# Performance work log

Measured on AMD Instinct MI355X. Metric: run time of the kernel, lower is better.

Reference implementation:

```python
import jax, jax.numpy as jnp
import numpy as np

NUM_HEADS = 16
HIDDEN = 1024
EPS = 1e-5


def _layernorm(x, g, b):
    mu = jnp.mean(x, axis=-1, keepdims=True)
    var = jnp.mean((x - mu) ** 2, axis=-1, keepdims=True)
    return (x - mu) * jax.lax.rsqrt(var + EPS) * g + b


def setup_inputs() -> dict:
    key = jax.random.key(0)
    ks = jax.random.split(key, 10)
    B, S, H = 2, 2048, HIDDEN
    s = 0.02
    d = {
        "X": jax.random.normal(ks[0], (B, S, H), jnp.float32),
        "Wq": jax.random.normal(ks[1], (H, H), jnp.float32) * s,
        "bq": jnp.zeros((H,), jnp.float32),
        "Wk": jax.random.normal(ks[2], (H, H), jnp.float32) * s,
        "bk": jnp.zeros((H,), jnp.float32),
        "Wv": jax.random.normal(ks[3], (H, H), jnp.float32) * s,
        "bv": jnp.zeros((H,), jnp.float32),
        "Wo": jax.random.normal(ks[4], (H, H), jnp.float32) * s,
        "bo": jnp.zeros((H,), jnp.float32),
        "ln1_g": jnp.ones((H,), jnp.float32),
        "ln1_b": jnp.zeros((H,), jnp.float32),
        "Wup": jax.random.normal(ks[5], (4 * H, H), jnp.float32) * s,
        "bup": jnp.zeros((4 * H,), jnp.float32),
        "Wdown": jax.random.normal(ks[6], (H, 4 * H), jnp.float32) * s,
        "bdown": jnp.zeros((H,), jnp.float32),
        "ln2_g": jnp.ones((H,), jnp.float32),
        "ln2_b": jnp.zeros((H,), jnp.float32),
    }
    return d


def reference(X, Wq, bq, Wk, bk, Wv, bv, Wo, bo, ln1_g, ln1_b,
              Wup, bup, Wdown, bdown, ln2_g, ln2_b):
    B, S, H = X.shape
    nh = NUM_HEADS
    hd = H // nh
    # QKV projections -> [B, nh, S, hd]
    q = (X @ Wq.T + bq).reshape(B, S, nh, hd).transpose(0, 2, 1, 3)
    k = (X @ Wk.T + bk).reshape(B, S, nh, hd).transpose(0, 2, 1, 3)
    v = (X @ Wv.T + bv).reshape(B, S, nh, hd).transpose(0, 2, 1, 3)
    scores = jnp.einsum("bhqd,bhkd->bhqk", q, k) / jnp.sqrt(jnp.float32(hd))
    causal = jnp.tril(jnp.ones((S, S), dtype=bool))
    scores = jnp.where(causal, scores, jnp.float32(-1e20))
    att = jax.nn.softmax(scores, axis=-1)  # dropout p=0 (eval)
    mid = jnp.einsum("bhqk,bhkd->bhqd", att, v)  # [B, nh, S, hd]
    mid = mid.transpose(0, 2, 1, 3).reshape(B, S, H)
    att_out = mid @ Wo.T + bo
    h = _layernorm(X + att_out, ln1_g, ln1_b)
    up = jax.nn.relu(h @ Wup.T + bup)
    down = up @ Wdown.T + bdown
    return _layernorm(h + down, ln2_g, ln2_b)
```

## Files before the change

### kernel.cpp

```cpp
#include <hip/hip_runtime.h>

#define B_ 2
#define S_ 2048
#define H_ 1024
#define NH 16
#define HD 64
#define LN_EPS 1e-5f

typedef unsigned short u16;
typedef unsigned int u32;
typedef __attribute__((ext_vector_type(8))) short bf16x8;
typedef __attribute__((ext_vector_type(4))) float f32x4;
typedef __attribute__((ext_vector_type(16))) float f32x16;
typedef __attribute__((ext_vector_type(4))) u32 u32x4;
typedef __attribute__((ext_vector_type(4))) u16 u16x4;

__device__ __forceinline__ u16 f2bf(float f) {
  u32 u = __float_as_uint(f);
  u32 r = (u + 0x7FFFu + ((u >> 16) & 1u)) >> 16;
  return (u16)r;
}
__device__ __forceinline__ float bflo(u32 w) { return __uint_as_float(w << 16); }
__device__ __forceinline__ float bfhi(u32 w) { return __uint_as_float(w & 0xffff0000u); }

__device__ __forceinline__ void gload_lds16(const void* g, void* l) {
  __builtin_amdgcn_global_load_lds(
      (const __attribute__((address_space(1))) void*)(uintptr_t)g,
      (__attribute__((address_space(3))) void*)(uintptr_t)l, 16, 0, 0);
}

__global__ __launch_bounds__(256) void k_cvt_all(const float* __restrict__ X,
                                                 const float* __restrict__ Wq,
                                                 const float* __restrict__ Wk,
                                                 const float* __restrict__ Wv,
                                                 const float* __restrict__ Wo,
                                                 const float* __restrict__ Wup,
                                                 const float* __restrict__ Wdn,
                                                 u16* __restrict__ dst) {
  const int i = blockIdx.x * 256 + threadIdx.x;
  const float* s;
  int off;
  if (i < 1048576)      { s = X;   off = 0; }
  else if (i < 1310720) { s = Wq;  off = 1048576; }
  else if (i < 1572864) { s = Wk;  off = 1310720; }
  else if (i < 1835008) { s = Wv;  off = 1572864; }
  else if (i < 2097152) { s = Wo;  off = 1835008; }
  else if (i < 3145728) { s = Wup; off = 2097152; }
  else                  { s = Wdn; off = 3145728; }
  f32x4 v = ((const f32x4*)s)[i - off];
  u16x4 o = { f2bf(v[0]), f2bf(v[1]), f2bf(v[2]), f2bf(v[3]) };
  ((u16x4*)dst)[i] = o;
}

__global__ __launch_bounds__(256) void k_pack3(const float* __restrict__ a,
                                               const float* __restrict__ b,
                                               const float* __restrict__ c,
                                               float* __restrict__ o) {
  int i = blockIdx.x * 256 + threadIdx.x;
  if (i >= 3 * H_) return;
  o[i] = (i < H_) ? a[i] : (i < 2 * H_ ? b[i - H_] : c[i - 2 * H_]);
}

template<int RELU, int F32OUT, int BF16OUT, int BIAS>
__global__ __launch_bounds__(512, 2) void k_gemm8(const u16* __restrict__ A,
                                                  const u16* __restrict__ W,
                                                  const float* __restrict__ bias,
                                                  float* __restrict__ outf,
                                                  u16* __restrict__ outb,
                                                  int M, int N, int lda, int ldb,
                                                  int Kc, int tilesM) {
  extern __shared__ u16 lds[];
  const int tid = threadIdx.x, lane = tid & 63, wid = tid >> 6;
  const int wr = wid >> 2, wc = wid & 3;
  const int lr = lane & 15, lk = lane >> 4;

  const int nwg = gridDim.x;
  const int bid = blockIdx.x;
  const int lid = (bid & 7) * (nwg >> 3) + (bid >> 3);
  const int ty = lid % tilesM;
  const int txz = lid / tilesM;
  const int tilesN = N >> 8;
  const int tx = txz % tilesN;
  const int kz = txz / tilesN;
  const int row0 = ty << 8, col0 = tx << 8;
  A += (size_t)kz * Kc;
  W += (size_t)kz * Kc;
  const size_t outoff = (size_t)kz * M * N;

  const int NT = Kc >> 6;

  f32x4 acc[8][4];
#pragma unroll
  for (int i = 0; i < 8; ++i)
#pragma unroll
    for (int j = 0; j < 4; ++j) acc[i][j] = (f32x4){0.f, 0.f, 0.f, 0.f};

  const int srow = tid >> 3;
  const int csw8 = ((tid & 7) ^ (srow & 7)) << 3;

  auto stage_ht = [&](int ht) {
    const int t = ht >> 2, sel = ht & 3;
    const int mat = (sel < 2) ? 1 : 0;
    const int hh = sel & 1;
    const u16* g = mat ? W : A;
    const int ld = mat ? ldb : lda;
    const int b0 = mat ? col0 : row0;
    const int kt = t << 6;
    u16* dst = lds + ((t & 1) << 15) + (mat << 14) + (hh << 13) + tid * 8;
#pragma unroll
    for (int j = 0; j < 2; ++j) {
      const int r = (hh << 7) + (j << 6) + srow;
      gload_lds16(g + (size_t)(b0 + r) * ld + kt + csw8, dst + (j << 12));
    }
  };

  union UU { u32x4 u; bf16x8 b; };
  auto ldvec = [&](const u16* base, int r, int c) -> bf16x8 {
    UU x;
    x.u = *(const u32x4*)(base + r * 64 + ((c ^ (r & 7)) << 3));
    return x.b;
  };

#pragma unroll
  for (int i = 0; i < 4; ++i) stage_ht(i);
  asm volatile("s_waitcnt vmcnt(0)" ::: "memory");
  __builtin_amdgcn_s_barrier();

  for (int t = 0; t < NT; ++t) {
    const u16* SA = lds + ((t & 1) << 15);
    const u16* SB = SA + 16384;
#pragma unroll
    for (int ph = 0; ph < 4; ++ph) {
      const int mh = ph >> 1, ks = ph & 1;
      const int c = (ks << 2) + lk;
      bf16x8 bb[4], aa[4];
#pragma unroll
      for (int ni = 0; ni < 4; ++ni)
        bb[ni] = ldvec(SB, (wc << 6) + (ni << 4) + lr, c);
#pragma unroll
      for (int mi = 0; mi < 4; ++mi)
        aa[mi] = ldvec(SA, (wr << 7) + (mh << 6) + (mi << 4) + lr, c);
      if (t + 1 < NT && ph < 2) {
        stage_ht(4 * (t + 1) + 2 * ph);
        stage_ht(4 * (t + 1) + 2 * ph + 1);
      }
      __builtin_amdgcn_s_barrier();
      __builtin_amdgcn_s_setprio(1);
#pragma unroll
      for (int mi = 0; mi < 4; ++mi)
#pragma unroll
        for (int ni = 0; ni < 4; ++ni)
          acc[(mh << 2) + mi][ni] = __builtin_amdgcn_mfma_f32_16x16x32_bf16(
              aa[mi], bb[ni], acc[(mh << 2) + mi][ni], 0, 0, 0);
      __builtin_amdgcn_s_setprio(0);
      if (ph == 3)
        asm volatile("s_waitcnt vmcnt(0)" ::: "memory");
      __builtin_amdgcn_s_barrier();
    }
  }

  float bs[4] = {0.f, 0.f, 0.f, 0.f};
  if (BIAS) {
#pragma unroll
    for (int ni = 0; ni < 4; ++ni)
      bs[ni] = bias[col0 + (wc << 6) + (ni << 4) + lr];
  }
#pragma unroll
  for (int mi = 0; mi < 8; ++mi) {
#pragma unroll
    for (int ni = 0; ni < 4; ++ni) {
#pragma unroll
      for (int r = 0; r < 4; ++r) {
        int row = row0 + (wr << 7) + (mi << 4) + (lk << 2) + r;
        int col = col0 + (wc << 6) + (ni << 4) + lr;
        float v = acc[mi][ni][r] + bs[ni];
        if (RELU) v = fmaxf(v, 0.f);
        if (F32OUT) outf[outoff + (size_t)row * N + col] = v;
        if (BF16OUT) outb[outoff + (size_t)row * N + col] = f2bf(v);
      }
    }
  }
}

__global__ __launch_bounds__(256) void k_vt(const u16* __restrict__ QKV,
                                            u16* __restrict__ vt) {
  __shared__ u16 T[64 * 64];
  const int tid = threadIdx.x;
  const int s0 = blockIdx.x * 64;
  const int bh = blockIdx.y;
  const int b = bh >> 4, h = bh & 15;
#pragma unroll
  for (int p = 0; p < 2; ++p) {
    int id = p * 256 + tid;
    int r = id >> 3, c = id & 7;
    u32x4 v = *(const u32x4*)(QKV + (size_t)(b * S_ + s0 + r) * 3072 + 2048 + h * 64 + c * 8);
    int sw = (r ^ (r >> 3)) & 7;
    *(u32x4*)(T + r * 64 + ((c ^ sw) << 3)) = v;
  }
  __syncthreads();
#pragma unroll
  for (int p = 0; p < 2; ++p) {
    int id = p * 256 + tid;
    int d = id >> 3, cs = id & 7;
    u16 tmp[8];
#pragma unroll
    for (int k = 0; k < 8; ++k) {
      int r = cs * 8 + k;
      int sw = (r ^ (r >> 3)) & 7;
      tmp[k] = T[r * 64 + ((((d >> 3) ^ sw)) << 3) + (d & 7)];
    }
    *(u32x4*)(vt + ((size_t)bh * 64 + d) * 2048 + s0 + cs * 8) = *(const u32x4*)tmp;
  }
}

__global__ __launch_bounds__(256, 3) void k_attn_mfma(const u16* __restrict__ QKV,
                                                      const u16* __restrict__ Vt,
                                                      u16* __restrict__ mid) {
  __shared__ u16 lds[9216];
  u16* Ks = lds;
  u16* Vs = lds + 4096;
  const int tid = threadIdx.x, lane = tid & 63, wid = tid >> 6;
  const int lq = lane & 31, lh = lane >> 5;
  const int qb = (S_ / 128 - 1) - blockIdx.x;
  const int bh = blockIdx.y;
  const int b = bh >> 4, h = bh & 15;
  const int q0w = qb * 128 + wid * 32;
  const int qg = q0w + lq;

  union U { u32x4 u; bf16x8 b; };
  U qf[4];
#pragma unroll
  for (int ks = 0; ks < 4; ++ks) {
    const size_t off = (size_t)(b * S_ + qg) * 3072 + h * HD + ks * 16 + lh * 8;
    u32x4 u = *(const u32x4*)(QKV + off);
    u32x4 s;
#pragma unroll
    for (int t = 0; t < 4; ++t) {
      u32 lo = (u32)f2bf(bflo(u[t]) * 0.125f);
      u32 hi = (u32)f2bf(bfhi(u[t]) * 0.125f);
      s[t] = lo | (hi << 16);
    }
    qf[ks].u = s;
  }

  float m = -1e30f, l = 0.f;
  f32x16 acc[2];
#pragma unroll
  for (int mo = 0; mo < 2; ++mo)
#pragma unroll
    for (int r = 0; r < 16; ++r) acc[mo][r] = 0.f;

  const int nt = qb * 2 + 2;
  for (int kv = 0; kv < nt; ++kv) {
    const int kv0 = kv * 64;
    __syncthreads();
#pragma unroll
    for (int p = 0; p < 2; ++p) {
      int id = p * 256 + tid;
      int r = id >> 3, c = id & 7;
      u32x4 ku = *(const u32x4*)(QKV + (size_t)(b * S_ + kv0 + r) * 3072 + 1024 + h * 64 + c * 8);
      *(u32x4*)(Ks + r * 64 + ((c ^ (r & 7)) << 3)) = ku;
      u32x4 vu = *(const u32x4*)(Vt + ((size_t)bh * 64 + r) * 2048 + kv0 + c * 8);
      *(u32x4*)(Vs + r * 64 + ((c ^ (r & 7)) << 3)) = vu;
    }
    __syncthreads();

    if (kv0 > q0w + 31) continue;

    f32x16 sf[2];
#pragma unroll
    for (int nf = 0; nf < 2; ++nf)
#pragma unroll
      for (int r = 0; r < 16; ++r) sf[nf][r] = 0.f;
    __builtin_amdgcn_s_setprio(1);
#pragma unroll
    for (int ks = 0; ks < 4; ++ks) {
#pragma unroll
      for (int nf = 0; nf < 2; ++nf) {
        int r = nf * 32 + lq;
        int c = ks * 2 + lh;
        U kf;
        kf.u = *(const u32x4*)(Ks + r * 64 + ((c ^ (r & 7)) << 3));
        sf[nf] = __builtin_amdgcn_mfma_f32_32x32x16_bf16(kf.b, qf[ks].b, sf[nf], 0, 0, 0);
      }
    }
    __builtin_amdgcn_s_setprio(0);

    if (kv0 + 63 > q0w) {
#pragma unroll
      for (int nf = 0; nf < 2; ++nf)
#pragma unroll
        for (int r = 0; r < 16; ++r) {
          int kvg = kv0 + nf * 32 + (r & 3) + 8 * (r >> 2) + 4 * lh;
          if (kvg > qg) sf[nf][r] = -1e30f;
        }
    }

    float tm = sf[0][0];
#pragma unroll
    for (int r = 1; r < 16; ++r) tm = fmaxf(tm, sf[0][r]);
#pragma unroll
    for (int r = 0; r < 16; ++r) tm = fmaxf(tm, sf[1][r]);
    tm = fmaxf(tm, __shfl_xor(tm, 32));
    if (__any(tm - m > 8.f)) {
      const float mn = fmaxf(m, tm);
      const float corr = __expf(m - mn);
      m = mn;
      l *= corr;
#pragma unroll
      for (int mo = 0; mo < 2; ++mo)
#pragma unroll
        for (int r = 0; r < 16; ++r) acc[mo][r] *= corr;
    }
    float rs = 0.f;
#pragma unroll
    for (int nf = 0; nf < 2; ++nf)
#pragma unroll
      for (int r = 0; r < 16; ++r) {
        float p = __expf(sf[nf][r] - m);
        sf[nf][r] = p;
        rs += p;
      }
    rs += __shfl_xor(rs, 32);
    l += rs;

    u32 q32[2][8];
#pragma unroll
    for (int nf = 0; nf < 2; ++nf)
#pragma unroll
      for (int i = 0; i < 8; ++i)
        asm("v_cvt_pk_bf16_f32 %0, %1, %2"
            : "=v"(q32[nf][i]) : "v"(sf[nf][2 * i]), "v"(sf[nf][2 * i + 1]));

    __builtin_amdgcn_s_setprio(1);
#pragma unroll
    for (int s = 0; s < 4; ++s) {
      const int nfp = s >> 1, sg = s & 1;
      u32 x = q32[nfp][4 * sg + 0];
      u32 y = q32[nfp][4 * sg + 1];
      u32 z = q32[nfp][4 * sg + 2];
      u32 w = q32[nfp][4 * sg + 3];
      asm("v_permlane32_swap_b32 %0, %1" : "+v"(x), "+v"(z));
      asm("v_permlane32_swap_b32 %0, %1" : "+v"(y), "+v"(w));
      U pb;
      pb.u = (u32x4){x, y, z, w};
#pragma unroll
      for (int mo = 0; mo < 2; ++mo) {
        int r = mo * 32 + lq;
        int c = s * 2 + lh;
        U vv;
        vv.u = *(const u32x4*)(Vs + r * 64 + ((c ^ (r & 7)) << 3));
        acc[mo] = __builtin_amdgcn_mfma_f32_32x32x16_bf16(vv.b, pb.b, acc[mo], 0, 0, 0);
      }
    }
    __builtin_amdgcn_s_setprio(0);
  }

  __syncthreads();
  u16* Ow = lds + wid * (32 * 72);
  const float inv = 1.f / l;
#pragma unroll
  for (int mo = 0; mo < 2; ++mo)
#pragma unroll
    for (int r = 0; r < 16; ++r) {
      int d = mo * 32 + (r & 3) + 8 * (r >> 2) + 4 * lh;
      Ow[lq * 72 + d] = f2bf(acc[mo][r] * inv);
    }
  __asm__ volatile("" ::: "memory");
#pragma unroll
  for (int r4 = 0; r4 < 4; ++r4) {
    int ql = r4 * 8 + (lane >> 3);
    int c = lane & 7;
    u32x4 v = *(const u32x4*)(Ow + ql * 72 + c * 8);
    *(u32x4*)(mid + (size_t)(b * S_ + q0w + ql) * H_ + h * HD + c * 8) = v;
  }
}

template<int BF16OUT, int NZ>
__global__ __launch_bounds__(256) void k_lnr(const float* __restrict__ a,
                                             const u16* __restrict__ P,
                                             const float* __restrict__ bd,
                                             const float* __restrict__ g,
                                             const float* __restrict__ bb,
                                             float* __restrict__ outf,
                                             u16* __restrict__ outb) {
  __shared__ float red[8];
  const int row = blockIdx.x, tid = threadIdx.x;
  const size_t base = (size_t)row * H_ + tid * 4;
  f32x4 t = *(const f32x4*)(a + base);
  f32x4 vb = *(const f32x4*)(bd + tid * 4);
  t += vb;
#pragma unroll
  for (int z = 0; z < NZ; ++z) {
    u16x4 p = *(const u16x4*)(P + (size_t)z * ((size_t)B_ * S_ * H_) + base);
#pragma unroll
    for (int e = 0; e < 4; ++e) t[e] += __uint_as_float((u32)p[e] << 16);
  }
  float sum = t[0] + t[1] + t[2] + t[3];
#pragma unroll
  for (int msk = 32; msk >= 1; msk >>= 1) sum += __shfl_xor(sum, msk, 64);
  if ((tid & 63) == 0) red[tid >> 6] = sum;
  __syncthreads();
  float mu = (red[0] + red[1] + red[2] + red[3]) * (1.f / H_);
  f32x4 d = t - mu;
  float sq = d[0] * d[0] + d[1] * d[1] + d[2] * d[2] + d[3] * d[3];
#pragma unroll
  for (int msk = 32; msk >= 1; msk >>= 1) sq += __shfl_xor(sq, msk, 64);
  if ((tid & 63) == 0) red[4 + (tid >> 6)] = sq;
  __syncthreads();
  float var = (red[4] + red[5] + red[6] + red[7]) * (1.f / H_);
  float rs = rsqrtf(var + LN_EPS);
  f32x4 gg = *(const f32x4*)(g + tid * 4);
  f32x4 bv = *(const f32x4*)(bb + tid * 4);
  f32x4 o = d * rs * gg + bv;
  *(f32x4*)(outf + base) = o;
  if (BF16OUT) {
    u16x4 ob = { f2bf(o[0]), f2bf(o[1]), f2bf(o[2]), f2bf(o[3]) };
    *(u16x4*)(outb + base) = ob;
  }
}

extern "C" void kernel_launch(void* const* d_in, const int* in_sizes, int n_in,
                              void* d_out, int out_size, void* d_ws, size_t ws_size,
                              hipStream_t stream) {
  const float* X   = (const float*)d_in[0];
  const float* Wq  = (const float*)d_in[1];
  const float* bq  = (const float*)d_in[2];
  const float* Wk  = (const float*)d_in[3];
  const float* bk  = (const float*)d_in[4];
  const float* Wv  = (const float*)d_in[5];
  const float* bv  = (const float*)d_in[6];
  const float* Wo  = (const float*)d_in[7];
  const float* bo  = (const float*)d_in[8];
  const float* g1  = (const float*)d_in[9];
  const float* b1  = (const float*)d_in[10];
  const float* Wup = (const float*)d_in[11];
  const float* bup = (const float*)d_in[12];
  const float* Wdn = (const float*)d_in[13];
  const float* bdn = (const float*)d_in[14];
  const float* g2  = (const float*)d_in[15];
  const float* b2  = (const float*)d_in[16];
  float* out = (float*)d_out;

  const size_t MS = (size_t)B_ * S_;
  const size_t nX = MS * H_;

  char* ws = (char*)d_ws;
  size_t off = 0;
  auto alloc = [&](size_t bytes) {
    char* p = ws + off;
    off += (bytes + 255) & ~(size_t)255;
    return p;
  };
  u16* Xb    = (u16*)alloc(nX * 2);
  u16* Wqkv  = (u16*)alloc((size_t)3 * H_ * H_ * 2);
  u16* Wob   = (u16*)alloc((size_t)H_ * H_ * 2);
  u16* Wupb  = (u16*)alloc((size_t)4 * H_ * H_ * 2);
  u16* Wdnb  = (u16*)alloc((size_t)4 * H_ * H_ * 2);
  float* bqkv = (float*)alloc(3 * H_ * 4);
  u16* QKVb  = (u16*)alloc(nX * 3 * 2);
  u16* midb  = (u16*)alloc(nX * 2);
  u16* Pbuf  = (u16*)alloc(nX * 4 * 2);
  float* h   = (float*)Xb;
  u16* upb   = QKVb;
  u16* vtb   = Pbuf;
  u16* WoP   = Pbuf;
  u16* hb    = Pbuf + nX * 2;
  u16* P     = Pbuf;

  dim3 blk(256);

  k_cvt_all<<<dim3(16384), blk, 0, stream>>>(X, Wq, Wk, Wv, Wo, Wup, Wdn, Xb);
  k_pack3<<<dim3(12), blk, 0, stream>>>(bq, bk, bv, bqkv);

  k_gemm8<0, 0, 1, 1><<<dim3(16 * 12), dim3(512), 131072, stream>>>(
      Xb, Wqkv, bqkv, nullptr, QKVb, (int)MS, 3 * H_, H_, H_, H_, 16);

  k_vt<<<dim3(S_ / 64, B_ * NH), blk, 0, stream>>>(QKVb, vtb);

  k_attn_mfma<<<dim3(S_ / 128, B_ * NH), blk, 0, stream>>>(QKVb, vtb, midb);

  k_gemm8<0, 0, 1, 0><<<dim3(16 * 4 * 2), dim3(512), 131072, stream>>>(
      midb, Wob, nullptr, nullptr, WoP, (int)MS, H_, H_, H_, 512, 16);

  k_lnr<1, 2><<<dim3(MS), blk, 0, stream>>>(X, WoP, bo, g1, b1, h, hb);

  k_gemm8<1, 0, 1, 1><<<dim3(16 * 16), dim3(512), 131072, stream>>>(
      hb, Wupb, bup, nullptr, upb, (int)MS, 4 * H_, H_, H_, H_, 16);

  k_gemm8<0, 0, 1, 0><<<dim3(16 * 4 * 4), dim3(512), 131072, stream>>>(
      upb, Wdnb, nullptr, nullptr, P, (int)MS, H_, 4 * H_, 4 * H_, H_, 16);

  k_lnr<0, 4><<<dim3(MS), blk, 0, stream>>>(h, P, bdn, g2, b2, out, nullptr);
}
```

Baseline: 231.4 us.

## Double-buffer K/V tiles in attention kernel with register prefetch

The attention kernel now keeps two LDS slots for K and V tiles. It issues global loads for the next KV tile into registers before computing on the current tile, then writes them to the other slot after compute, which removes one barrier per iteration. This targets global-load latency that previously sat exposed between the barrier pair. In exchange, LDS use grows from 18 KB to 32 KB and the occupancy hint of 3 blocks is dropped, so register and LDS pressure may reduce resident waves.

```diff
diff --git a/kernel.cpp b/kernel.cpp
--- a/kernel.cpp
+++ b/kernel.cpp
@@ -213,12 +213,10 @@
   }
 }
 
-__global__ __launch_bounds__(256, 3) void k_attn_mfma(const u16* __restrict__ QKV,
-                                                      const u16* __restrict__ Vt,
-                                                      u16* __restrict__ mid) {
-  __shared__ u16 lds[9216];
-  u16* Ks = lds;
-  u16* Vs = lds + 4096;
+__global__ __launch_bounds__(256) void k_attn_mfma(const u16* __restrict__ QKV,
+                                                   const u16* __restrict__ Vt,
+                                                   u16* __restrict__ mid) {
+  __shared__ u16 lds[16384];
   const int tid = threadIdx.x, lane = tid & 63, wid = tid >> 6;
   const int lq = lane & 31, lh = lane >> 5;
   const int qb = (S_ / 128 - 1) - blockIdx.x;
@@ -251,112 +249,135 @@
     for (int r = 0; r < 16; ++r) acc[mo][r] = 0.f;
 
   const int nt = qb * 2 + 2;
-  for (int kv = 0; kv < nt; ++kv) {
-    const int kv0 = kv * 64;
-    __syncthreads();
+
+  u32x4 kreg[2], vreg[2];
+  auto issue = [&](int kv) {
 #pragma unroll
     for (int p = 0; p < 2; ++p) {
       int id = p * 256 + tid;
       int r = id >> 3, c = id & 7;
-      u32x4 ku = *(const u32x4*)(QKV + (size_t)(b * S_ + kv0 + r) * 3072 + 1024 + h * 64 + c * 8);
-      *(u32x4*)(Ks + r * 64 + ((c ^ (r & 7)) << 3)) = ku;
-      u32x4 vu = *(const u32x4*)(Vt + ((size_t)bh * 64 + r) * 2048 + kv0 + c * 8);
-      *(u32x4*)(Vs + r * 64 + ((c ^ (r & 7)) << 3)) = vu;
-    }
+      kreg[p] = *(const u32x4*)(QKV + (size_t)(b * S_ + kv * 64 + r) * 3072 + 1024 + h * 64 + c * 8);
+      vreg[p] = *(const u32x4*)(Vt + ((size_t)bh * 64 + r) * 2048 + kv * 64 + c * 8);
+    }
+  };
+  auto store = [&](int slot) {
+    u16* Ks = lds + slot * 8192;
+    u16* Vs = Ks + 4096;
+#pragma unroll
+    for (int p = 0; p < 2; ++p) {
+      int id = p * 256 + tid;
+      int r = id >> 3, c = id & 7;
+      *(u32x4*)(Ks + r * 64 + ((c ^ (r & 7)) << 3)) = kreg[p];
+      *(u32x4*)(Vs + r * 64 + ((c ^ (r & 7)) << 3)) = vreg[p];
+    }
+  };
+
+  issue(0);
+  store(0);
+  __syncthreads();
+
+  for (int kv = 0; kv < nt; ++kv) {
+    const int kv0 = kv * 64;
+    const int cur = kv & 1;
+    if (kv + 1 < nt) issue(kv + 1);
+
+    if (kv0 <= q0w + 31) {
+      const u16* Ks = lds + cur * 8192;
+      const u16* Vs = Ks + 4096;
+
+      f32x16 sf[2];
+#pragma unroll
+      for (int nf = 0; nf < 2; ++nf)
+#pragma unroll
+        for (int r = 0; r < 16; ++r) sf[nf][r] = 0.f;
+      __builtin_amdgcn_s_setprio(1);
+#pragma unroll
+      for (int ks = 0; ks < 4; ++ks) {
+#pragma unroll
+        for (int nf = 0; nf < 2; ++nf) {
+          int r = nf * 32 + lq;
+          int c = ks * 2 + lh;
+          U kf;
+          kf.u = *(const u32x4*)(Ks + r * 64 + ((c ^ (r & 7)) << 3));
+          sf[nf] = __builtin_amdgcn_mfma_f32_32x32x16_bf16(kf.b, qf[ks].b, sf[nf], 0, 0, 0);
+        }
+      }
+      __builtin_amdgcn_s_setprio(0);
+
+      if (kv0 + 63 > q0w) {
+#pragma unroll
+        for (int nf = 0; nf < 2; ++nf)
+#pragma unroll
+          for (int r = 0; r < 16; ++r) {
+            int kvg = kv0 + nf * 32 + (r & 3) + 8 * (r >> 2) + 4 * lh;
+            if (kvg > qg) sf[nf][r] = -1e30f;
+          }
+      }
+
+      float tm = sf[0][0];
+#pragma unroll
+      for (int r = 1; r < 16; ++r) tm = fmaxf(tm, sf[0][r]);
+#pragma unroll
+      for (int r = 0; r < 16; ++r) tm = fmaxf(tm, sf[1][r]);
+      tm = fmaxf(tm, __shfl_xor(tm, 32));
+      if (__any(tm - m > 8.f)) {
+        const float mn = fmaxf(m, tm);
+        const float corr = __expf(m - mn);
+        m = mn;
+        l *= corr;
+#pragma unroll
+        for (int mo = 0; mo < 2; ++mo)
+#pragma unroll
+          for (int r = 0; r < 16; ++r) acc[mo][r] *= corr;
+      }
+      float rs = 0.f;
+#pragma unroll
+      for (int nf = 0; nf < 2; ++nf)
+#pragma unroll
+        for (int r = 0; r < 16; ++r) {
+          float p = __expf(sf[nf][r] - m);
+          sf[nf][r] = p;
+          rs += p;
+        }
+      rs += __shfl_xor(rs, 32);
+      l += rs;
+
+      u32 q32[2][8];
+#pragma unroll
+      for (int nf = 0; nf < 2; ++nf)
+#pragma unroll
+        for (int i = 0; i < 8; ++i)
+          asm("v_cvt_pk_bf16_f32 %0, %1, %2"
+              : "=v"(q32[nf][i]) : "v"(sf[nf][2 * i]), "v"(sf[nf][2 * i + 1]));
+
+      __builtin_amdgcn_s_setprio(1);
+#pragma unroll
+      for (int s = 0; s < 4; ++s) {
+        const int nfp = s >> 1, sg = s & 1;
+        u32 x = q32[nfp][4 * sg + 0];
+        u32 y = q32[nfp][4 * sg + 1];
+        u32 z = q32[nfp][4 * sg + 2];
+        u32 w = q32[nfp][4 * sg + 3];
+        asm("v_permlane32_swap_b32 %0, %1" : "+v"(x), "+v"(z));
+        asm("v_permlane32_swap_b32 %0, %1" : "+v"(y), "+v"(w));
+        U pb;
+        pb.u = (u32x4){x, y, z, w};
+#pragma unroll
+        for (int mo = 0; mo < 2; ++mo) {
+          int r = mo * 32 + lq;
+          int c = s * 2 + lh;
+          U vv;
+          vv.u = *(const u32x4*)(Vs + r * 64 + ((c ^ (r & 7)) << 3));
+          acc[mo] = __builtin_amdgcn_mfma_f32_32x32x16_bf16(vv.b, pb.b, acc[mo], 0, 0, 0);
+        }
+      }
+      __builtin_amdgcn_s_setprio(0);
+    }
+
+    if (kv + 1 < nt) store(cur ^ 1);
     __syncthreads();
-
-    if (kv0 > q0w + 31) continue;
-
-    f32x16 sf[2];
-#pragma unroll
-    for (int nf = 0; nf < 2; ++nf)
-#pragma unroll
-      for (int r = 0; r < 16; ++r) sf[nf][r] = 0.f;
-    __builtin_amdgcn_s_setprio(1);
-#pragma unroll
-    for (int ks = 0; ks < 4; ++ks) {
-#pragma unroll
-      for (int nf = 0; nf < 2; ++nf) {
-        int r = nf * 32 + lq;
-        int c = ks * 2 + lh;
-        U kf;
-        kf.u = *(const u32x4*)(Ks + r * 64 + ((c ^ (r & 7)) << 3));
-        sf[nf] = __builtin_amdgcn_mfma_f32_32x32x16_bf16(kf.b, qf[ks].b, sf[nf], 0, 0, 0);
-      }
-    }
-    __builtin_amdgcn_s_setprio(0);
-
-    if (kv0 + 63 > q0w) {
-#pragma unroll
-      for (int nf = 0; nf < 2; ++nf)
-#pragma unroll
-        for (int r = 0; r < 16; ++r) {
-          int kvg = kv0 + nf * 32 + (r & 3) + 8 * (r >> 2) + 4 * lh;
-          if (kvg > qg) sf[nf][r] = -1e30f;
-        }
-    }
-
-    float tm = sf[0][0];
-#pragma unroll
-    for (int r = 1; r < 16; ++r) tm = fmaxf(tm, sf[0][r]);
-#pragma unroll
-    for (int r = 0; r < 16; ++r) tm = fmaxf(tm, sf[1][r]);
-    tm = fmaxf(tm, __shfl_xor(tm, 32));
-    if (__any(tm - m > 8.f)) {
-      const float mn = fmaxf(m, tm);
-      const float corr = __expf(m - mn);
-      m = mn;
-      l *= corr;
-#pragma unroll
-      for (int mo = 0; mo < 2; ++mo)
-#pragma unroll
-        for (int r = 0; r < 16; ++r) acc[mo][r] *= corr;
-    }
-    float rs = 0.f;
-#pragma unroll
-    for (int nf = 0; nf < 2; ++nf)
-#pragma unroll
-      for (int r = 0; r < 16; ++r) {
-        float p = __expf(sf[nf][r] - m);
-        sf[nf][r] = p;
-        rs += p;
-      }
-    rs += __shfl_xor(rs, 32);
-    l += rs;
-
-    u32 q32[2][8];
-#pragma unroll
-    for (int nf = 0; nf < 2; ++nf)
-#pragma unroll
-      for (int i = 0; i < 8; ++i)
-        asm("v_cvt_pk_bf16_f32 %0, %1, %2"
-            : "=v"(q32[nf][i]) : "v"(sf[nf][2 * i]), "v"(sf[nf][2 * i + 1]));
-
-    __builtin_amdgcn_s_setprio(1);
-#pragma unroll
-    for (int s = 0; s < 4; ++s) {
-      const int nfp = s >> 1, sg = s & 1;
-      u32 x = q32[nfp][4 * sg + 0];
-      u32 y = q32[nfp][4 * sg + 1];
-      u32 z = q32[nfp][4 * sg + 2];
-      u32 w = q32[nfp][4 * sg + 3];
-      asm("v_permlane32_swap_b32 %0, %1" : "+v"(x), "+v"(z));
-      asm("v_permlane32_swap_b32 %0, %1" : "+v"(y), "+v"(w));
-      U pb;
-      pb.u = (u32x4){x, y, z, w};
-#pragma unroll
-      for (int mo = 0; mo < 2; ++mo) {
-        int r = mo * 32 + lq;
-        int c = s * 2 + lh;
-        U vv;
-        vv.u = *(const u32x4*)(Vs + r * 64 + ((c ^ (r & 7)) << 3));
-        acc[mo] = __builtin_amdgcn_mfma_f32_32x32x16_bf16(vv.b, pb.b, acc[mo], 0, 0, 0);
-      }
-    }
-    __builtin_amdgcn_s_setprio(0);
-  }
-
-  __syncthreads();
+  }
+
   u16* Ow = lds + wid * (32 * 72);
   const float inv = 1.f / l;
 #pragma unroll
```

New measurement: 234.5 us. Within noise of the previous version (+1.4%).
